# Kernel tuning notes

Hardware: AMD Instinct MI355X
Metric: run time of the kernel (lower is better)

The kernel has to match this reference:

```python
import jax, jax.numpy as jnp
import numpy as np

N_NODES = 100000
N_EDGES = 1600000
IN_FEATS = 128
HEADS = 4
OUT_FEATS = 16
NEG_SLOPE = 0.2  # DGL GATConv default negative_slope


def setup_inputs() -> dict:
    key = jax.random.key(0)
    ks = jax.random.split(key, 7)
    feats = jax.random.normal(ks[0], (N_NODES, IN_FEATS), dtype=jnp.float32)
    W = jax.random.normal(ks[1], (HEADS * OUT_FEATS, IN_FEATS), dtype=jnp.float32) * 0.05
    attn_l = jax.random.normal(ks[2], (HEADS, OUT_FEATS), dtype=jnp.float32) * 0.1
    attn_r = jax.random.normal(ks[3], (HEADS, OUT_FEATS), dtype=jnp.float32) * 0.1
    bias = jax.random.normal(ks[4], (HEADS * OUT_FEATS,), dtype=jnp.float32) * 0.01
    src = jax.random.randint(ks[5], (N_EDGES,), 0, N_NODES, dtype=jnp.int64 if jax.config.jax_enable_x64 else jnp.int32)
    dst = jax.random.randint(ks[6], (N_EDGES,), 0, N_NODES, dtype=jnp.int64 if jax.config.jax_enable_x64 else jnp.int32)
    return {"feats": feats, "W": W, "attn_l": attn_l, "attn_r": attn_r,
            "bias": bias, "src": src, "dst": dst}


def reference(feats, W, attn_l, attn_r, bias, src, dst):
    """GATConv forward on a homogeneous graph built from concatenated edge lists.

    feats: [N, in_feats]; W: [H*F, in_feats]; attn_l/attn_r: [H, F]; bias: [H*F]
    src/dst: [E] edge endpoint indices. Returns [N, H, F] (DGL GATConv output).
    """
    N = feats.shape[0]
    H, F = attn_l.shape
    # Linear projection, per-head split: z [N, H, F]
    z = (feats @ W.T).reshape(N, H, F)
    # Per-node attention logits: el/er [N, H]
    el = jnp.einsum('nhf,hf->nh', z, attn_l)
    er = jnp.einsum('nhf,hf->nh', z, attn_r)
    # Per-edge unnormalized attention: e [E, H]
    e = jax.nn.leaky_relu(el[src] + er[dst], negative_slope=NEG_SLOPE)
    # Edge softmax over incoming edges of each destination node
    m = jax.ops.segment_max(e, dst, num_segments=N)           # [N, H]
    m = jnp.where(jnp.isfinite(m), m, jnp.zeros_like(m))      # guard empty segments
    ex = jnp.exp(e - m[dst])                                  # [E, H]
    denom = jax.ops.segment_sum(ex, dst, num_segments=N)      # [N, H]
    alpha = ex / denom[dst]                                   # [E, H]
    # Weighted message aggregation: scatter-add z[src] * alpha into dst
    msg = z[src] * alpha[:, :, None]                          # [E, H, F]
    out = jax.ops.segment_sum(msg, dst, num_segments=N)       # [N, H, F]
    return out + bias.reshape(1, H, F)
```

## Files before the change

### kernel.cpp

```cpp
#include <hip/hip_runtime.h>

#define N_NODES 100000
#define N_EDGES 1600000
#define IN_F    128
#define HEADS   4
#define OUT_F   16
#define HF      64
#define NEG_SLOPE 0.2f
#define NB_MFMA 1563

#define BUCK    112
#define NBUCK   893
#define BSTRIDE 2048
#define BSC_CHUNK 6144
#define NB_BSC  261
#define BUCK3   56
#define K3_BLOCKS 1786

typedef __attribute__((ext_vector_type(8))) short short8;
typedef __attribute__((ext_vector_type(4))) float f32x4;

__device__ __forceinline__ short f2bf(float f) {
    union { float f; unsigned u; } v; v.f = f;
    return (short)((v.u + 0x7FFFu + ((v.u >> 16) & 1u)) >> 16);
}

__global__ __launch_bounds__(256) void k_prep(const float* __restrict__ W,
                                              const float* __restrict__ attn_l,
                                              const float* __restrict__ attn_r,
                                              unsigned short* __restrict__ Wfrag,
                                              int* __restrict__ gcur) {
    __shared__ float Bext[16 * IN_F];
    int t = threadIdx.x;
    for (int i = t; i < NBUCK; i += 256) gcur[i] = 0;
    for (int o = t; o < 16 * IN_F; o += 256) {
        int c = o >> 7, k = o & 127;
        float v = 0.f;
        if (c < 8) {
            int hh = c & 3;
            const float* at = (c < 4) ? attn_l : attn_r;
            #pragma unroll
            for (int f = 0; f < 16; ++f)
                v += W[(size_t)(hh * 16 + f) * IN_F + k] * at[hh * 16 + f];
        }
        Bext[o] = v;
    }
    __syncthreads();
    for (int idx = t; idx < 20 * 64 * 8; idx += 256) {
        int j = idx & 7;
        int lane = (idx >> 3) & 63;
        int g = idx >> 9;
        int ct = g >> 2, kf = g & 3;
        int n = lane & 15, qq = lane >> 4;
        int k = kf * 32 + qq * 8 + j;
        float val = (ct < 4) ? W[(size_t)(ct * 16 + n) * IN_F + k]
                             : Bext[n * IN_F + k];
        Wfrag[idx] = (unsigned short)f2bf(val);
    }
}

__global__ __launch_bounds__(256) void k1_mfma(const float* __restrict__ feats,
                                               const unsigned short* __restrict__ Wfrag,
                                               unsigned short* __restrict__ zb,
                                               float* __restrict__ el,
                                               float* __restrict__ er) {
    const int t = threadIdx.x;
    const int grp = t >> 6;
    const int l = t & 63;
    const int q = l >> 4, n = l & 15;

    short8 bfrag[5][4];
    #pragma unroll
    for (int ct = 0; ct < 5; ++ct)
        #pragma unroll
        for (int kf = 0; kf < 4; ++kf)
            bfrag[ct][kf] = *(const short8*)(Wfrag + (size_t)((ct * 4 + kf) * 64 + l) * 8);

    int anode = blockIdx.x * 64 + grp * 16 + n;
    int aclamp = anode < N_NODES ? anode : 0;
    const float* arow = feats + (size_t)aclamp * IN_F + q * 8;

    f32x4 acc[5];
    #pragma unroll
    for (int ct = 0; ct < 5; ++ct) acc[ct] = (f32x4){0.f, 0.f, 0.f, 0.f};

    #pragma unroll
    for (int kf = 0; kf < 4; ++kf) {
        float4 x = *(const float4*)(arow + kf * 32);
        float4 y = *(const float4*)(arow + kf * 32 + 4);
        short8 a;
        a[0] = f2bf(x.x); a[1] = f2bf(x.y); a[2] = f2bf(x.z); a[3] = f2bf(x.w);
        a[4] = f2bf(y.x); a[5] = f2bf(y.y); a[6] = f2bf(y.z); a[7] = f2bf(y.w);
        #pragma unroll
        for (int ct = 0; ct < 5; ++ct)
            acc[ct] = __builtin_amdgcn_mfma_f32_16x16x32_bf16(a, bfrag[ct][kf], acc[ct], 0, 0, 0);
    }

    #pragma unroll
    for (int reg = 0; reg < 4; ++reg) {
        int onode = blockIdx.x * 64 + grp * 16 + q * 4 + reg;
        if (onode >= N_NODES) continue;
        #pragma unroll
        for (int ct = 0; ct < 4; ++ct)
            zb[(size_t)onode * HF + ct * 16 + n] = (unsigned short)f2bf(acc[ct][reg]);
        float v4 = acc[4][reg];
        if (n < 4)       el[onode * HEADS + n] = v4;
        else if (n < 8)  er[onode * HEADS + (n - 4)] = v4;
    }
}

__global__ __launch_bounds__(1024) void k_bsc(const int* __restrict__ src,
                                              const int* __restrict__ dst,
                                              int* __restrict__ gcur,
                                              unsigned* __restrict__ bin) {
    __shared__ int h[NBUCK], cur[NBUCK];
    const int t = threadIdx.x;
    if (t < NBUCK) { h[t] = 0; }
    __syncthreads();
    const int start = blockIdx.x * BSC_CHUNK;
    int end = start + BSC_CHUNK;
    if (end > N_EDGES) end = N_EDGES;

    int myd[6];
    #pragma unroll
    for (int k = 0; k < 6; ++k) {
        int i = start + t + k * 1024;
        myd[k] = (i < end) ? dst[i] : -1;
        if (myd[k] >= 0) atomicAdd(&h[(unsigned)myd[k] / BUCK], 1);
    }
    __syncthreads();
    if (t < NBUCK) cur[t] = h[t] ? atomicAdd(&gcur[t], h[t]) : 0;
    __syncthreads();
    #pragma unroll
    for (int k = 0; k < 6; ++k) {
        int i = start + t + k * 1024;
        if (i < end) {
            unsigned d = (unsigned)myd[k];
            unsigned b = d / BUCK;
            unsigned dl = d - b * BUCK;
            int pos = atomicAdd(&cur[b], 1);
            if (pos < BSTRIDE)
                bin[(size_t)b * BSTRIDE + pos] = (unsigned)src[i] | (dl << 17);
        }
    }
}

__global__ __launch_bounds__(256) void k3_sort(const unsigned* __restrict__ bin,
                                               const int* __restrict__ gcur,
                                               const float* __restrict__ el,
                                               const float* __restrict__ er,
                                               const unsigned short* __restrict__ zb,
                                               const float* __restrict__ bias,
                                               float* __restrict__ out) {
    __shared__ unsigned raw[BSTRIDE];
    __shared__ unsigned sorted[BSTRIDE];
    __shared__ int hist[BUCK3];
    __shared__ int noff[BUCK3 + 1];
    __shared__ int cur[BUCK3];
    __shared__ int s[64];
    __shared__ float er_s[BUCK3 * HEADS];

    const int t = threadIdx.x;
    const int B2 = blockIdx.x >> 1;
    const int half = blockIdx.x & 1;
    const int dlo = half * BUCK3;
    const int nodebase = B2 * BUCK + dlo;
    const unsigned* mybin = bin + (size_t)B2 * BSTRIDE;
    int cnt = gcur[B2];
    if (cnt > BSTRIDE) cnt = BSTRIDE;

    if (t < BUCK3) hist[t] = 0;
    if (t < BUCK3 * HEADS) {
        int g = nodebase * HEADS + t;
        er_s[t] = (g < N_NODES * HEADS) ? er[g] : 0.f;
    }
    for (int i = t; i < cnt; i += 256) raw[i] = mybin[i];
    __syncthreads();

    for (int i = t; i < cnt; i += 256) {
        int d2 = (int)(raw[i] >> 17) - dlo;
        if ((unsigned)d2 < BUCK3) atomicAdd(&hist[d2], 1);
    }
    __syncthreads();

    if (t < 64) s[t] = (t < BUCK3) ? hist[t] : 0;
    __syncthreads();
    for (int o = 1; o < 64; o <<= 1) {
        int x = (t < 64 && t >= o) ? s[t - o] : 0;
        __syncthreads();
        if (t < 64) s[t] += x;
        __syncthreads();
    }
    if (t < BUCK3) {
        int excl = s[t] - hist[t];
        noff[t] = excl;
        cur[t] = excl;
    }
    if (t == 0) noff[BUCK3] = s[BUCK3 - 1];
    __syncthreads();

    for (int i = t; i < cnt; i += 256) {
        unsigned p = raw[i];
        int d2 = (int)(p >> 17) - dlo;
        if ((unsigned)d2 < BUCK3) {
            int pos = atomicAdd(&cur[d2], 1);
            sorted[pos] = p & 0x1FFFF;
        }
    }
    __syncthreads();

    const int wave = t >> 6, lane = t & 63;
    const int j = lane >> 3;
    const int c = lane & 7;
    const int h = c >> 1;

    for (int nl = wave; nl < BUCK3; nl += 4) {
        int node = nodebase + nl;
        if (node >= N_NODES) break;
        const int nlo = noff[nl], nhi = noff[nl + 1];
        const float er_d = er_s[nl * HEADS + h];

        float4 A0 = make_float4(0.f, 0.f, 0.f, 0.f);
        float4 A1 = make_float4(0.f, 0.f, 0.f, 0.f);
        float den = 0.f;
        for (int i = nlo + j; i < nhi; i += 8) {
            int sN = sorted[i];
            float x = el[sN * HEADS + h] + er_d;
            x = x > 0.f ? x : NEG_SLOPE * x;
            float ex = __expf(x);
            den += ex;
            uint4 v = *(const uint4*)(zb + (size_t)sN * HF + c * 8);
            A0.x += ex * __uint_as_float(v.x << 16);
            A0.y += ex * __uint_as_float(v.x & 0xFFFF0000u);
            A0.z += ex * __uint_as_float(v.y << 16);
            A0.w += ex * __uint_as_float(v.y & 0xFFFF0000u);
            A1.x += ex * __uint_as_float(v.z << 16);
            A1.y += ex * __uint_as_float(v.z & 0xFFFF0000u);
            A1.z += ex * __uint_as_float(v.w << 16);
            A1.w += ex * __uint_as_float(v.w & 0xFFFF0000u);
        }
        #pragma unroll
        for (int m = 8; m <= 32; m <<= 1) {
            A0.x += __shfl_xor(A0.x, m); A0.y += __shfl_xor(A0.y, m);
            A0.z += __shfl_xor(A0.z, m); A0.w += __shfl_xor(A0.w, m);
            A1.x += __shfl_xor(A1.x, m); A1.y += __shfl_xor(A1.y, m);
            A1.z += __shfl_xor(A1.z, m); A1.w += __shfl_xor(A1.w, m);
            den  += __shfl_xor(den,  m);
        }
        if (j == 0) {
            float4 b0 = *(const float4*)(bias + c * 8);
            float4 b1 = *(const float4*)(bias + c * 8 + 4);
            if (den > 0.f) {
                float inv = 1.f / den;
                b0.x += A0.x * inv; b0.y += A0.y * inv;
                b0.z += A0.z * inv; b0.w += A0.w * inv;
                b1.x += A1.x * inv; b1.y += A1.y * inv;
                b1.z += A1.z * inv; b1.w += A1.w * inv;
            }
            *(float4*)(out + (size_t)node * HF + c * 8) = b0;
            *(float4*)(out + (size_t)node * HF + c * 8 + 4) = b1;
        }
    }
}

extern "C" void kernel_launch(void* const* d_in, const int* in_sizes, int n_in,
                              void* d_out, int out_size, void* d_ws, size_t ws_size,
                              hipStream_t stream) {
    const float* feats  = (const float*)d_in[0];
    const float* W      = (const float*)d_in[1];
    const float* attn_l = (const float*)d_in[2];
    const float* attn_r = (const float*)d_in[3];
    const float* bias   = (const float*)d_in[4];
    const int*   src    = (const int*)d_in[5];
    const int*   dst    = (const int*)d_in[6];
    float* out = (float*)d_out;

    char* ws = (char*)d_ws;
    unsigned short* zb = (unsigned short*)ws;  ws += (size_t)N_NODES * HF * 2;
    float* el    = (float*)ws;                 ws += N_NODES * HEADS * 4;
    float* er    = (float*)ws;                 ws += N_NODES * HEADS * 4;
    unsigned short* Wfrag = (unsigned short*)ws; ws += 20 * 64 * 8 * 2;
    int*   gcur  = (int*)ws;                   ws += 1024 * 4;
    unsigned* bin = (unsigned*)ws;             ws += (size_t)NBUCK * BSTRIDE * 4;

    k_prep  <<<1,         256,  0, stream>>>(W, attn_l, attn_r, Wfrag, gcur);
    k1_mfma <<<NB_MFMA,   256,  0, stream>>>(feats, Wfrag, zb, el, er);
    k_bsc   <<<NB_BSC,    1024, 0, stream>>>(src, dst, gcur, bin);
    k3_sort <<<K3_BLOCKS, 256,  0, stream>>>(bin, gcur, el, er, zb, bias, out);
}
```

Measured before the change: 194.1 us.

## Fuse projection and edge bucketing into one launch, precompute fp16 edge exps

The edge-bucketing scatter now runs inside the MFMA projection kernel, with every seventh block doing the binning, so both independent stages share one launch and overlap. The prep kernel is spread over 24 blocks, which drops its shared-memory staging. The sort kernel reads the bin straight from global memory instead of staging a raw copy in LDS. It also computes all four heads' exp logits once per edge during the scatter and stores them as fp16 in LDS, where before each lane recomputed them in the aggregation loop. In exchange, per-node edge storage is capped at SCAP (1408) entries, which risks dropping edges in unusually dense buckets, and fp16 exps lose some precision.

```diff
diff --git a/kernel.cpp b/kernel.cpp
--- a/kernel.cpp
+++ b/kernel.cpp
@@ -16,6 +16,9 @@
 #define NB_BSC  261
 #define BUCK3   56
 #define K3_BLOCKS 1786
+#define SCAP    1408
+
+#define NB_FUSED 1827
 
 typedef __attribute__((ext_vector_type(8))) short short8;
 typedef __attribute__((ext_vector_type(4))) float f32x4;
@@ -30,41 +33,85 @@
                                               const float* __restrict__ attn_r,
                                               unsigned short* __restrict__ Wfrag,
                                               int* __restrict__ gcur) {
-    __shared__ float Bext[16 * IN_F];
-    int t = threadIdx.x;
-    for (int i = t; i < NBUCK; i += 256) gcur[i] = 0;
-    for (int o = t; o < 16 * IN_F; o += 256) {
-        int c = o >> 7, k = o & 127;
-        float v = 0.f;
-        if (c < 8) {
-            int hh = c & 3;
-            const float* at = (c < 4) ? attn_l : attn_r;
+    const int g = blockIdx.x, t = threadIdx.x;
+    if (g >= 20) {
+        int i = (g - 20) * 256 + t;
+        if (i < 1024) gcur[i] = 0;
+        return;
+    }
+    const int ct = g >> 2, kf = g & 3;
+    #pragma unroll
+    for (int e = 0; e < 2; ++e) {
+        int off = e * 256 + t;
+        int j = off & 7, lane = off >> 3;
+        int n = lane & 15, qq = lane >> 4;
+        int k = kf * 32 + qq * 8 + j;
+        float v;
+        if (ct < 4) {
+            v = W[(size_t)(ct * 16 + n) * IN_F + k];
+        } else if (n < 8) {
+            int hh = n & 3;
+            const float* at = (n < 4) ? attn_l : attn_r;
+            v = 0.f;
             #pragma unroll
             for (int f = 0; f < 16; ++f)
                 v += W[(size_t)(hh * 16 + f) * IN_F + k] * at[hh * 16 + f];
-        }
-        Bext[o] = v;
-    }
-    __syncthreads();
-    for (int idx = t; idx < 20 * 64 * 8; idx += 256) {
-        int j = idx & 7;
-        int lane = (idx >> 3) & 63;
-        int g = idx >> 9;
-        int ct = g >> 2, kf = g & 3;
-        int n = lane & 15, qq = lane >> 4;
-        int k = kf * 32 + qq * 8 + j;
-        float val = (ct < 4) ? W[(size_t)(ct * 16 + n) * IN_F + k]
-                             : Bext[n * IN_F + k];
-        Wfrag[idx] = (unsigned short)f2bf(val);
-    }
-}
-
-__global__ __launch_bounds__(256) void k1_mfma(const float* __restrict__ feats,
+        } else {
+            v = 0.f;
+        }
+        Wfrag[(size_t)g * 512 + off] = (unsigned short)f2bf(v);
+    }
+}
+
+__global__ __launch_bounds__(256) void k_fused(const float* __restrict__ feats,
                                                const unsigned short* __restrict__ Wfrag,
                                                unsigned short* __restrict__ zb,
                                                float* __restrict__ el,
-                                               float* __restrict__ er) {
+                                               float* __restrict__ er,
+                                               const int* __restrict__ src,
+                                               const int* __restrict__ dst,
+                                               int* __restrict__ gcur,
+                                               unsigned* __restrict__ bin) {
+    const unsigned bx = blockIdx.x;
+    const unsigned q7 = bx / 7u, r7 = bx % 7u;
     const int t = threadIdx.x;
+
+    if (r7 == 6u) {
+        __shared__ int h[NBUCK], cur[NBUCK];
+        for (int i = t; i < NBUCK; i += 256) h[i] = 0;
+        __syncthreads();
+        const int start = (int)q7 * BSC_CHUNK;
+        int end = start + BSC_CHUNK;
+        if (end > N_EDGES) end = N_EDGES;
+
+        int myd[24];
+        #pragma unroll
+        for (int k = 0; k < 24; ++k) {
+            int i = start + t + k * 256;
+            myd[k] = (i < end) ? dst[i] : -1;
+            if (myd[k] >= 0) atomicAdd(&h[(unsigned)myd[k] / BUCK], 1);
+        }
+        __syncthreads();
+        for (int i = t; i < NBUCK; i += 256) cur[i] = h[i] ? atomicAdd(&gcur[i], h[i]) : 0;
+        __syncthreads();
+        #pragma unroll
+        for (int k = 0; k < 24; ++k) {
+            int i = start + t + k * 256;
+            if (i < end) {
+                unsigned d = (unsigned)myd[k];
+                unsigned b = d / BUCK;
+                unsigned dl = d - b * BUCK;
+                int pos = atomicAdd(&cur[b], 1);
+                if (pos < BSTRIDE)
+                    bin[(size_t)b * BSTRIDE + pos] = (unsigned)src[i] | (dl << 17);
+            }
+        }
+        return;
+    }
+
+    const int bid = (int)(bx - q7);
+    if (bid >= NB_MFMA) return;
+
     const int grp = t >> 6;
     const int l = t & 63;
     const int q = l >> 4, n = l & 15;
@@ -76,7 +123,7 @@
         for (int kf = 0; kf < 4; ++kf)
             bfrag[ct][kf] = *(const short8*)(Wfrag + (size_t)((ct * 4 + kf) * 64 + l) * 8);
 
-    int anode = blockIdx.x * 64 + grp * 16 + n;
+    int anode = bid * 64 + grp * 16 + n;
     int aclamp = anode < N_NODES ? anode : 0;
     const float* arow = feats + (size_t)aclamp * IN_F + q * 8;
 
@@ -98,7 +145,7 @@
 
     #pragma unroll
     for (int reg = 0; reg < 4; ++reg) {
-        int onode = blockIdx.x * 64 + grp * 16 + q * 4 + reg;
+        int onode = bid * 64 + grp * 16 + q * 4 + reg;
         if (onode >= N_NODES) continue;
         #pragma unroll
         for (int ct = 0; ct < 4; ++ct)
@@ -106,42 +153,6 @@
         float v4 = acc[4][reg];
         if (n < 4)       el[onode * HEADS + n] = v4;
         else if (n < 8)  er[onode * HEADS + (n - 4)] = v4;
-    }
-}
-
-__global__ __launch_bounds__(1024) void k_bsc(const int* __restrict__ src,
-                                              const int* __restrict__ dst,
-                                              int* __restrict__ gcur,
-                                              unsigned* __restrict__ bin) {
-    __shared__ int h[NBUCK], cur[NBUCK];
-    const int t = threadIdx.x;
-    if (t < NBUCK) { h[t] = 0; }
-    __syncthreads();
-    const int start = blockIdx.x * BSC_CHUNK;
-    int end = start + BSC_CHUNK;
-    if (end > N_EDGES) end = N_EDGES;
-
-    int myd[6];
-    #pragma unroll
-    for (int k = 0; k < 6; ++k) {
-        int i = start + t + k * 1024;
-        myd[k] = (i < end) ? dst[i] : -1;
-        if (myd[k] >= 0) atomicAdd(&h[(unsigned)myd[k] / BUCK], 1);
-    }
-    __syncthreads();
-    if (t < NBUCK) cur[t] = h[t] ? atomicAdd(&gcur[t], h[t]) : 0;
-    __syncthreads();
-    #pragma unroll
-    for (int k = 0; k < 6; ++k) {
-        int i = start + t + k * 1024;
-        if (i < end) {
-            unsigned d = (unsigned)myd[k];
-            unsigned b = d / BUCK;
-            unsigned dl = d - b * BUCK;
-            int pos = atomicAdd(&cur[b], 1);
-            if (pos < BSTRIDE)
-                bin[(size_t)b * BSTRIDE + pos] = (unsigned)src[i] | (dl << 17);
-        }
     }
 }
 
@@ -152,8 +163,8 @@
                                                const unsigned short* __restrict__ zb,
                                                const float* __restrict__ bias,
                                                float* __restrict__ out) {
-    __shared__ unsigned raw[BSTRIDE];
-    __shared__ unsigned sorted[BSTRIDE];
+    __shared__ unsigned sorted[SCAP];
+    __shared__ __align__(8) unsigned short exs[SCAP*4];
     __shared__ int hist[BUCK3];
     __shared__ int noff[BUCK3 + 1];
     __shared__ int cur[BUCK3];
@@ -174,11 +185,10 @@
         int g = nodebase * HEADS + t;
         er_s[t] = (g < N_NODES * HEADS) ? er[g] : 0.f;
     }
-    for (int i = t; i < cnt; i += 256) raw[i] = mybin[i];
     __syncthreads();
 
     for (int i = t; i < cnt; i += 256) {
-        int d2 = (int)(raw[i] >> 17) - dlo;
+        int d2 = (int)(mybin[i] >> 17) - dlo;
         if ((unsigned)d2 < BUCK3) atomicAdd(&hist[d2], 1);
     }
     __syncthreads();
@@ -200,11 +210,30 @@
     __syncthreads();
 
     for (int i = t; i < cnt; i += 256) {
-        unsigned p = raw[i];
+        unsigned p = mybin[i];
         int d2 = (int)(p >> 17) - dlo;
         if ((unsigned)d2 < BUCK3) {
             int pos = atomicAdd(&cur[d2], 1);
-            sorted[pos] = p & 0x1FFFF;
+            if (pos < SCAP) {
+                int sN = (int)(p & 0x1FFFF);
+                float4 e4 = *(const float4*)(el + (size_t)sN * HEADS);
+                float x0 = e4.x + er_s[d2 * HEADS + 0];
+                float x1 = e4.y + er_s[d2 * HEADS + 1];
+                float x2 = e4.z + er_s[d2 * HEADS + 2];
+                float x3 = e4.w + er_s[d2 * HEADS + 3];
+                x0 = x0 > 0.f ? x0 : NEG_SLOPE * x0;
+                x1 = x1 > 0.f ? x1 : NEG_SLOPE * x1;
+                x2 = x2 > 0.f ? x2 : NEG_SLOPE * x2;
+                x3 = x3 > 0.f ? x3 : NEG_SLOPE * x3;
+                unsigned short q0 = __builtin_bit_cast(unsigned short, (_Float16)__expf(x0));
+                unsigned short q1 = __builtin_bit_cast(unsigned short, (_Float16)__expf(x1));
+                unsigned short q2 = __builtin_bit_cast(unsigned short, (_Float16)__expf(x2));
+                unsigned short q3 = __builtin_bit_cast(unsigned short, (_Float16)__expf(x3));
+                sorted[pos] = (unsigned)sN;
+                *(uint2*)(exs + pos * 4) =
+                    make_uint2((unsigned)q0 | ((unsigned)q1 << 16),
+                               (unsigned)q2 | ((unsigned)q3 << 16));
+            }
         }
     }
     __syncthreads();
@@ -217,19 +246,17 @@
     for (int nl = wave; nl < BUCK3; nl += 4) {
         int node = nodebase + nl;
         if (node >= N_NODES) break;
-        const int nlo = noff[nl], nhi = noff[nl + 1];
-        const float er_d = er_s[nl * HEADS + h];
+        int nlo = noff[nl], nhi = noff[nl + 1];
+        if (nhi > SCAP) nhi = SCAP;
 
         float4 A0 = make_float4(0.f, 0.f, 0.f, 0.f);
         float4 A1 = make_float4(0.f, 0.f, 0.f, 0.f);
         float den = 0.f;
         for (int i = nlo + j; i < nhi; i += 8) {
-            int sN = sorted[i];
-            float x = el[sN * HEADS + h] + er_d;
-            x = x > 0.f ? x : NEG_SLOPE * x;
-            float ex = __expf(x);
+            int sN = (int)sorted[i];
+            float ex = (float)__builtin_bit_cast(_Float16, exs[i * 4 + h]);
+            uint4 v = *(const uint4*)(zb + (size_t)sN * HF + c * 8);
             den += ex;
-            uint4 v = *(const uint4*)(zb + (size_t)sN * HF + c * 8);
             A0.x += ex * __uint_as_float(v.x << 16);
             A0.y += ex * __uint_as_float(v.x & 0xFFFF0000u);
             A0.z += ex * __uint_as_float(v.y << 16);
@@ -283,8 +310,7 @@
     int*   gcur  = (int*)ws;                   ws += 1024 * 4;
     unsigned* bin = (unsigned*)ws;             ws += (size_t)NBUCK * BSTRIDE * 4;
 
-    k_prep  <<<1,         256,  0, stream>>>(W, attn_l, attn_r, Wfrag, gcur);
-    k1_mfma <<<NB_MFMA,   256,  0, stream>>>(feats, Wfrag, zb, el, er);
-    k_bsc   <<<NB_BSC,    1024, 0, stream>>>(src, dst, gcur, bin);
-    k3_sort <<<K3_BLOCKS, 256,  0, stream>>>(bin, gcur, el, er, zb, bias, out);
-}
+    k_prep  <<<24,        256, 0, stream>>>(W, attn_l, attn_r, Wfrag, gcur);
+    k_fused <<<NB_FUSED,  256, 0, stream>>>(feats, Wfrag, zb, el, er, src, dst, gcur, bin);
+    k3_sort <<<K3_BLOCKS, 256, 0, stream>>>(bin, gcur, el, er, zb, bias, out);
+}
```

Result: slower. 204.5 us (+5.4%).
